# Performance work log

Measured on AMD Instinct MI355X. Metric: run time of the kernel, lower is better.

## Reference

```python
import jax, jax.numpy as jnp
import numpy as np
import math

B, T, D, H = 4, 2048, 1024, 16
HD = D // H  # head dim = 64

def setup_inputs() -> dict:
    key = jax.random.key(0)
    ks = jax.random.split(key, 4)
    scale = 1.0 / math.sqrt(D)
    return {
        "x": jax.random.normal(ks[0], (B, T, D), dtype=jnp.float32),
        "Wq": jax.random.normal(ks[1], (D, D), dtype=jnp.float32) * scale,
        "bq": jnp.zeros((D,), dtype=jnp.float32),
        "Wk": jax.random.normal(ks[2], (D, D), dtype=jnp.float32) * scale,
        "bk": jnp.zeros((D,), dtype=jnp.float32),
        "Wv": jax.random.normal(ks[3], (D, D), dtype=jnp.float32) * scale,
        "bv": jnp.zeros((D,), dtype=jnp.float32),
    }

def reference(x, Wq, bq, Wk, bk, Wv, bv):
    b, t, d = x.shape
    # QKV projections (nn.Dense): x @ W + b
    q = x @ Wq + bq
    k = x @ Wk + bk
    v = x @ Wv + bv
    # b n (h d) -> b h n d
    def split_heads(y):
        return y.reshape(b, t, H, HD).transpose(0, 2, 1, 3)
    q, k, v = split_heads(q), split_heads(k), split_heads(v)
    # scaled dot-product attention; scale by sqrt(features // heads)
    scores = jnp.einsum("bhqd,bhkd->bhqk", q, k) / math.sqrt(HD)
    attn = jax.nn.softmax(scores, axis=-1)
    # dropout rate 0.0 / eval mode => identity
    out = jnp.einsum("bhqk,bhkd->bhqd", attn, v)
    # b h n d -> b n (h d)
    return out.transpose(0, 2, 1, 3).reshape(b, t, d)
```

## Files before the change

### kernel.cpp

```cpp
#include <hip/hip_runtime.h>
#include <math.h>

typedef unsigned short u16;
typedef short short8 __attribute__((ext_vector_type(8)));
typedef short short4v __attribute__((ext_vector_type(4)));
typedef u16 u16x4 __attribute__((ext_vector_type(4)));
typedef float f32x4 __attribute__((ext_vector_type(4)));
typedef __bf16 bf16x8 __attribute__((ext_vector_type(8)));
typedef __bf16 bf16x4 __attribute__((ext_vector_type(4)));

#define B_ 4
#define T_ 2048
#define D_ 1024
#define H_ 16
#define HD_ 64
#define BT_ 8192

__device__ __forceinline__ u16 f2bf(float f) {
  unsigned u = __builtin_bit_cast(unsigned, f);
  u = u + 0x7fffu + ((u >> 16) & 1u);
  return (u16)(u >> 16);
}
__device__ __forceinline__ f32x4 mfma16(short8 a, short8 b, f32x4 c) {
  return __builtin_amdgcn_mfma_f32_16x16x32_bf16(
      __builtin_bit_cast(bf16x8, a), __builtin_bit_cast(bf16x8, b), c, 0, 0, 0);
}
#if __has_builtin(__builtin_amdgcn_mfma_f32_16x16x16bf16_1k)
__device__ __forceinline__ f32x4 mfma_pv(short4v p, short4v v, f32x4 c) {
  return __builtin_amdgcn_mfma_f32_16x16x16bf16_1k(
      __builtin_bit_cast(bf16x4, p), __builtin_bit_cast(bf16x4, v), c, 0, 0, 0);
}
#else
__device__ __forceinline__ f32x4 mfma_pv(short4v p, short4v v, f32x4 c) {
  short8 a = {p[0], p[1], p[2], p[3], 0, 0, 0, 0};
  short8 b = {v[0], v[1], v[2], v[3], 0, 0, 0, 0};
  return mfma16(a, b, c);
}
#endif
__device__ __forceinline__ void async16(u16* lds, const u16* g) {
  __builtin_amdgcn_global_load_lds(
      (const __attribute__((address_space(1))) unsigned int*)g,
      (__attribute__((address_space(3))) unsigned int*)lds, 16, 0, 0);
}
__device__ __forceinline__ short4v pack4(float p0, float p1, float p2, float p3) {
  bf16x4 t = {(__bf16)p0, (__bf16)p1, (__bf16)p2, (__bf16)p3};
  return __builtin_bit_cast(short4v, t);
}

__global__ __launch_bounds__(256) void convert_x(const float* __restrict__ in,
                                                 u16* __restrict__ out) {
  int i = (blockIdx.x * 256 + threadIdx.x) * 4;
  float4 v = *(const float4*)&in[i];
  u16x4 o = {f2bf(v.x), f2bf(v.y), f2bf(v.z), f2bf(v.w)};
  *(u16x4*)&out[i] = o;
}

__global__ __launch_bounds__(256) void transposeW3(
    const float* __restrict__ Wq, const float* __restrict__ Wk,
    const float* __restrict__ Wv, u16* __restrict__ wtq, u16* __restrict__ wtk,
    u16* __restrict__ wtv) {
  __shared__ float sh[32][33];
  const int wsel = blockIdx.y >> 5;
  const float* in = (wsel == 0) ? Wq : (wsel == 1) ? Wk : Wv;
  u16* out = (wsel == 0) ? wtq : (wsel == 1) ? wtk : wtv;
  const int bx = blockIdx.x * 32, by = (blockIdx.y & 31) * 32;
  const int col = threadIdx.x & 31, r8 = threadIdx.x >> 5;
#pragma unroll
  for (int i = 0; i < 4; i++) {
    int row = r8 + i * 8;
    sh[row][col] = in[(size_t)(by + row) * 1024 + bx + col];
  }
  __syncthreads();
#pragma unroll
  for (int i = 0; i < 4; i++) {
    int row = r8 + i * 8;
    out[(size_t)(bx + row) * 1024 + by + col] = f2bf(sh[col][row]);
  }
}

__global__ __launch_bounds__(256, 3) void gemm_qkv3(
    const u16* __restrict__ xbf, const u16* __restrict__ wtq,
    const u16* __restrict__ wtk, const u16* __restrict__ wtv,
    const float* __restrict__ bq, const float* __restrict__ bk,
    const float* __restrict__ bv, u16* __restrict__ qh, u16* __restrict__ kh,
    u16* __restrict__ vth, float qscale) {
  __shared__ __align__(16) u16 Rs[128 * 64];
  __shared__ __align__(16) u16 Cs[128 * 64];
  const int proj = blockIdx.y >> 3;
  const int fy = blockIdx.y & 7;
  const u16* Rm;
  const u16* Cm;
  const float* bias;
  u16* out;
  float scale;
  int r0, c0, vmode;
  if (proj == 0) {
    Rm = wtq; Cm = xbf; bias = bq; out = qh; scale = qscale; vmode = 0;
    r0 = fy * 128; c0 = blockIdx.x * 128;
  } else if (proj == 1) {
    Rm = wtk; Cm = xbf; bias = bk; out = kh; scale = 1.0f; vmode = 0;
    r0 = fy * 128; c0 = blockIdx.x * 128;
  } else {
    Rm = xbf; Cm = wtv; bias = bv; out = vth; scale = 1.0f; vmode = 1;
    r0 = blockIdx.x * 128; c0 = fy * 128;
  }
  const int tid = threadIdx.x;
  const int lane = tid & 63;
  const int w = tid >> 6;
  const int wr = w >> 1, wc = w & 1;
  const int c = lane & 15, q4 = lane >> 4;
  const int cx7 = c & 7;

  f32x4 acc[4][4];
#pragma unroll
  for (int i = 0; i < 4; i++)
#pragma unroll
    for (int j = 0; j < 4; j++) {
      f32x4 z = {0.f, 0.f, 0.f, 0.f};
      acc[i][j] = z;
    }

  const int sr = tid >> 3, pc = tid & 7;

  for (int kk = 0; kk < 1024; kk += 64) {
    __syncthreads();
#pragma unroll
    for (int i = 0; i < 4; i++) {
      int row = i * 32 + sr;
      int sc = (pc ^ (row & 7)) * 8;
      async16(&Rs[(i * 256 + tid) * 8], &Rm[(size_t)(r0 + row) * 1024 + kk + sc]);
      async16(&Cs[(i * 256 + tid) * 8], &Cm[(size_t)(c0 + row) * 1024 + kk + sc]);
    }
    __syncthreads();
#pragma unroll
    for (int h = 0; h < 2; h++) {
      short8 rF[4], cF[4];
      const int ko = ((h * 4 + q4) ^ cx7) * 8;
#pragma unroll
      for (int i = 0; i < 4; i++)
        rF[i] = *(const short8*)&Rs[(wr * 64 + i * 16 + c) * 64 + ko];
#pragma unroll
      for (int j = 0; j < 4; j++)
        cF[j] = *(const short8*)&Cs[(wc * 64 + j * 16 + c) * 64 + ko];
#pragma unroll
      for (int i = 0; i < 4; i++)
#pragma unroll
        for (int j = 0; j < 4; j++) acc[i][j] = mfma16(rF[i], cF[j], acc[i][j]);
    }
  }

  if (vmode == 0) {
#pragma unroll
    for (int i = 0; i < 4; i++) {
      int ng = r0 + wr * 64 + i * 16 + q4 * 4;
      int h = ng >> 6, hd = ng & 63;
#pragma unroll
      for (int j = 0; j < 4; j++) {
        int tg = c0 + wc * 64 + j * 16 + c;
        int b = tg >> 11, tt = tg & 2047;
        u16x4 o;
#pragma unroll
        for (int r = 0; r < 4; r++)
          o[r] = f2bf((acc[i][j][r] + bias[ng + r]) * scale);
        *(u16x4*)&out[(((size_t)(b * 16 + h) * 2048 + tt) << 6) + hd] = o;
      }
    }
  } else {
#pragma unroll
    for (int i = 0; i < 4; i++) {
      int tg = r0 + wr * 64 + i * 16 + q4 * 4;
      int b = tg >> 11, tt = tg & 2047;
#pragma unroll
      for (int j = 0; j < 4; j++) {
        int ng = c0 + wc * 64 + j * 16 + c;
        int h = ng >> 6, hd = ng & 63;
        float bb = bias[ng];
        u16x4 o;
#pragma unroll
        for (int r = 0; r < 4; r++) o[r] = f2bf(acc[i][j][r] + bb);
        *(u16x4*)&out[((size_t)((b * 16 + h) * 64 + hd)) * 2048 + tt] = o;
      }
    }
  }
}

__global__ __launch_bounds__(256, 4) void attn_fused(const u16* __restrict__ Qh,
                                                     const u16* __restrict__ Kh,
                                                     const u16* __restrict__ VTh,
                                                     float* __restrict__ out) {
  __shared__ __align__(16) u16 Ks[2][64 * 64];
  __shared__ __align__(16) u16 VTs[2][64 * 64];
  const int tid = threadIdx.x;
  const int w = tid >> 6, lane = tid & 63;
  const int c = lane & 15, q4 = lane >> 4;
  const int cx7 = c & 7;
  const int qt = blockIdx.x, bh = blockIdx.y;

  short8 qf[2][2];
#pragma unroll
  for (int nblk = 0; nblk < 2; nblk++) {
    const u16* Qp =
        Qh + ((size_t)bh * T_ + qt * 128 + w * 32 + nblk * 16 + c) * 64;
    qf[nblk][0] = *(const short8*)&Qp[q4 * 8];
    qf[nblk][1] = *(const short8*)&Qp[32 + q4 * 8];
  }

  const u16* Kb = Kh + (size_t)bh * T_ * 64;
  const u16* Vb = VTh + (size_t)bh * 64 * T_;

  f32x4 O[2][4];
#pragma unroll
  for (int nblk = 0; nblk < 2; nblk++)
#pragma unroll
    for (int nb = 0; nb < 4; nb++) {
      f32x4 z = {0.f, 0.f, 0.f, 0.f};
      O[nblk][nb] = z;
    }
  float lsum[2] = {0.f, 0.f};

  const int sr = tid >> 3, pc = tid & 7;

#pragma unroll
  for (int i = 0; i < 2; i++) {
    int r = i * 32 + sr;
    int sc = (pc ^ (r & 7)) * 8;
    async16(&Ks[0][(i * 256 + tid) * 8], &Kb[(size_t)r * 64 + sc]);
    async16(&VTs[0][(i * 256 + tid) * 8], &Vb[(size_t)r * T_ + sc]);
  }

  for (int it = 0; it < T_ / 64; it++) {
    const int cur = it & 1;
    __syncthreads();
    if (it + 1 < T_ / 64) {
      const int kt = (it + 1) * 64;
#pragma unroll
      for (int i = 0; i < 2; i++) {
        int r = i * 32 + sr;
        int sc = (pc ^ (r & 7)) * 8;
        async16(&Ks[cur ^ 1][(i * 256 + tid) * 8],
                &Kb[(size_t)(kt + r) * 64 + sc]);
        async16(&VTs[cur ^ 1][(i * 256 + tid) * 8],
                &Vb[(size_t)r * T_ + kt + sc]);
      }
    }

    f32x4 S[4][2];
#pragma unroll
    for (int kb = 0; kb < 4; kb++) {
      short8 k0 =
          *(const short8*)&Ks[cur][(kb * 16 + c) * 64 + ((q4 ^ cx7) * 8)];
      short8 k1 =
          *(const short8*)&Ks[cur][(kb * 16 + c) * 64 + (((4 + q4) ^ cx7) * 8)];
#pragma unroll
      for (int nblk = 0; nblk < 2; nblk++) {
        f32x4 z = {0.f, 0.f, 0.f, 0.f};
        S[kb][nblk] = mfma16(k0, qf[nblk][0], z);
        S[kb][nblk] = mfma16(k1, qf[nblk][1], S[kb][nblk]);
      }
    }

    short4v pf[2][4];
#pragma unroll
    for (int nblk = 0; nblk < 2; nblk++) {
      float rs = 0.f;
#pragma unroll
      for (int kb = 0; kb < 4; kb++) {
        float p0 = __builtin_amdgcn_exp2f(S[kb][nblk][0]);
        float p1 = __builtin_amdgcn_exp2f(S[kb][nblk][1]);
        float p2 = __builtin_amdgcn_exp2f(S[kb][nblk][2]);
        float p3 = __builtin_amdgcn_exp2f(S[kb][nblk][3]);
        rs += (p0 + p1) + (p2 + p3);
        pf[nblk][kb] = pack4(p0, p1, p2, p3);
      }
      lsum[nblk] += rs;
    }

#pragma unroll
    for (int kb = 0; kb < 4; kb++) {
      int pch = ((kb * 2 + (q4 >> 1)) ^ cx7) * 8 + (q4 & 1) * 4;
#pragma unroll
      for (int nb = 0; nb < 4; nb++) {
        short4v vf = *(const short4v*)&VTs[cur][(nb * 16 + c) * 64 + pch];
        O[0][nb] = mfma_pv(pf[0][kb], vf, O[0][nb]);
        O[1][nb] = mfma_pv(pf[1][kb], vf, O[1][nb]);
      }
    }
  }

#pragma unroll
  for (int nblk = 0; nblk < 2; nblk++) {
    lsum[nblk] += __shfl_xor(lsum[nblk], 16);
    lsum[nblk] += __shfl_xor(lsum[nblk], 32);
  }

  const int bq = bh >> 4, h = bh & 15;
#pragma unroll
  for (int nblk = 0; nblk < 2; nblk++)
#pragma unroll
    for (int r = 0; r < 4; r++) {
      float rl = 1.0f / __shfl(lsum[nblk], q4 * 4 + r);
      int t = qt * 128 + w * 32 + nblk * 16 + q4 * 4 + r;
#pragma unroll
      for (int nb = 0; nb < 4; nb++)
        out[((size_t)(bq * T_ + t)) * 1024 + h * 64 + nb * 16 + c] =
            O[nblk][nb][r] * rl;
    }
}

extern "C" void kernel_launch(void* const* d_in, const int* in_sizes, int n_in,
                              void* d_out, int out_size, void* d_ws, size_t ws_size,
                              hipStream_t stream) {
  (void)in_sizes; (void)n_in; (void)out_size; (void)ws_size;
  const float* x  = (const float*)d_in[0];
  const float* Wq = (const float*)d_in[1];
  const float* bq = (const float*)d_in[2];
  const float* Wk = (const float*)d_in[3];
  const float* bk = (const float*)d_in[4];
  const float* Wv = (const float*)d_in[5];
  const float* bv = (const float*)d_in[6];
  float* out = (float*)d_out;

  u16* ob  = (u16*)d_out;
  u16* xbf = ob;
  u16* wtq = ob + (size_t)BT_ * D_;
  u16* wtk = wtq + (size_t)D_ * D_;
  u16* wtv = wtk + (size_t)D_ * D_;

  u16* ws  = (u16*)d_ws;
  u16* qh  = ws;
  u16* kh  = qh + (size_t)BT_ * D_;
  u16* vth = kh + (size_t)BT_ * D_;

  convert_x<<<8192, 256, 0, stream>>>(x, xbf);
  transposeW3<<<dim3(32, 96), 256, 0, stream>>>(Wq, Wk, Wv, wtq, wtk, wtv);

  const float qscale = 0.125f * 1.44269504088896f;
  gemm_qkv3<<<dim3(64, 24), 256, 0, stream>>>(xbf, wtq, wtk, wtv, bq, bk, bv,
                                              qh, kh, vth, qscale);

  attn_fused<<<dim3(16, 64), 256, 0, stream>>>(qh, kh, vth, out);
}
```

Before: 263.7 us.

## Double query rows per attention block and use K=32 MFMA for PV

```diff
diff --git a/kernel.cpp b/kernel.cpp
--- a/kernel.cpp
+++ b/kernel.cpp
@@ -3,11 +3,9 @@
 
 typedef unsigned short u16;
 typedef short short8 __attribute__((ext_vector_type(8)));
-typedef short short4v __attribute__((ext_vector_type(4)));
 typedef u16 u16x4 __attribute__((ext_vector_type(4)));
 typedef float f32x4 __attribute__((ext_vector_type(4)));
 typedef __bf16 bf16x8 __attribute__((ext_vector_type(8)));
-typedef __bf16 bf16x4 __attribute__((ext_vector_type(4)));
 
 #define B_ 4
 #define T_ 2048
@@ -25,26 +23,10 @@
   return __builtin_amdgcn_mfma_f32_16x16x32_bf16(
       __builtin_bit_cast(bf16x8, a), __builtin_bit_cast(bf16x8, b), c, 0, 0, 0);
 }
-#if __has_builtin(__builtin_amdgcn_mfma_f32_16x16x16bf16_1k)
-__device__ __forceinline__ f32x4 mfma_pv(short4v p, short4v v, f32x4 c) {
-  return __builtin_amdgcn_mfma_f32_16x16x16bf16_1k(
-      __builtin_bit_cast(bf16x4, p), __builtin_bit_cast(bf16x4, v), c, 0, 0, 0);
-}
-#else
-__device__ __forceinline__ f32x4 mfma_pv(short4v p, short4v v, f32x4 c) {
-  short8 a = {p[0], p[1], p[2], p[3], 0, 0, 0, 0};
-  short8 b = {v[0], v[1], v[2], v[3], 0, 0, 0, 0};
-  return mfma16(a, b, c);
-}
-#endif
 __device__ __forceinline__ void async16(u16* lds, const u16* g) {
   __builtin_amdgcn_global_load_lds(
       (const __attribute__((address_space(1))) unsigned int*)g,
       (__attribute__((address_space(3))) unsigned int*)lds, 16, 0, 0);
-}
-__device__ __forceinline__ short4v pack4(float p0, float p1, float p2, float p3) {
-  bf16x4 t = {(__bf16)p0, (__bf16)p1, (__bf16)p2, (__bf16)p3};
-  return __builtin_bit_cast(short4v, t);
 }
 
 __global__ __launch_bounds__(256) void convert_x(const float* __restrict__ in,
@@ -170,6 +152,7 @@
     for (int i = 0; i < 4; i++) {
       int tg = r0 + wr * 64 + i * 16 + q4 * 4;
       int b = tg >> 11, tt = tg & 2047;
+      int tp = (tt & ~63) | (((tt >> 2) & 3) << 4) | (((tt >> 4) & 3) << 2);
 #pragma unroll
       for (int j = 0; j < 4; j++) {
         int ng = c0 + wc * 64 + j * 16 + c;
@@ -178,13 +161,13 @@
         u16x4 o;
 #pragma unroll
         for (int r = 0; r < 4; r++) o[r] = f2bf(acc[i][j][r] + bb);
-        *(u16x4*)&out[((size_t)((b * 16 + h) * 64 + hd)) * 2048 + tt] = o;
-      }
-    }
-  }
-}
-
-__global__ __launch_bounds__(256, 4) void attn_fused(const u16* __restrict__ Qh,
+        *(u16x4*)&out[((size_t)((b * 16 + h) * 64 + hd)) * 2048 + tp] = o;
+      }
+    }
+  }
+}
+
+__global__ __launch_bounds__(256, 2) void attn_fused(const u16* __restrict__ Qh,
                                                      const u16* __restrict__ Kh,
                                                      const u16* __restrict__ VTh,
                                                      float* __restrict__ out) {
@@ -196,11 +179,11 @@
   const int cx7 = c & 7;
   const int qt = blockIdx.x, bh = blockIdx.y;
 
-  short8 qf[2][2];
-#pragma unroll
-  for (int nblk = 0; nblk < 2; nblk++) {
+  short8 qf[4][2];
+#pragma unroll
+  for (int nblk = 0; nblk < 4; nblk++) {
     const u16* Qp =
-        Qh + ((size_t)bh * T_ + qt * 128 + w * 32 + nblk * 16 + c) * 64;
+        Qh + ((size_t)bh * T_ + qt * 256 + w * 64 + nblk * 16 + c) * 64;
     qf[nblk][0] = *(const short8*)&Qp[q4 * 8];
     qf[nblk][1] = *(const short8*)&Qp[32 + q4 * 8];
   }
@@ -208,15 +191,15 @@
   const u16* Kb = Kh + (size_t)bh * T_ * 64;
   const u16* Vb = VTh + (size_t)bh * 64 * T_;
 
-  f32x4 O[2][4];
-#pragma unroll
-  for (int nblk = 0; nblk < 2; nblk++)
+  f32x4 O[4][4];
+#pragma unroll
+  for (int nblk = 0; nblk < 4; nblk++)
 #pragma unroll
     for (int nb = 0; nb < 4; nb++) {
       f32x4 z = {0.f, 0.f, 0.f, 0.f};
       O[nblk][nb] = z;
     }
-  float lsum[2] = {0.f, 0.f};
+  float lsum[4] = {0.f, 0.f, 0.f, 0.f};
 
   const int sr = tid >> 3, pc = tid & 7;
 
@@ -244,62 +227,64 @@
       }
     }
 
-    f32x4 S[4][2];
-#pragma unroll
-    for (int kb = 0; kb < 4; kb++) {
-      short8 k0 =
-          *(const short8*)&Ks[cur][(kb * 16 + c) * 64 + ((q4 ^ cx7) * 8)];
-      short8 k1 =
-          *(const short8*)&Ks[cur][(kb * 16 + c) * 64 + (((4 + q4) ^ cx7) * 8)];
-#pragma unroll
-      for (int nblk = 0; nblk < 2; nblk++) {
-        f32x4 z = {0.f, 0.f, 0.f, 0.f};
-        S[kb][nblk] = mfma16(k0, qf[nblk][0], z);
-        S[kb][nblk] = mfma16(k1, qf[nblk][1], S[kb][nblk]);
-      }
-    }
-
-    short4v pf[2][4];
-#pragma unroll
-    for (int nblk = 0; nblk < 2; nblk++) {
-      float rs = 0.f;
-#pragma unroll
-      for (int kb = 0; kb < 4; kb++) {
-        float p0 = __builtin_amdgcn_exp2f(S[kb][nblk][0]);
-        float p1 = __builtin_amdgcn_exp2f(S[kb][nblk][1]);
-        float p2 = __builtin_amdgcn_exp2f(S[kb][nblk][2]);
-        float p3 = __builtin_amdgcn_exp2f(S[kb][nblk][3]);
-        rs += (p0 + p1) + (p2 + p3);
-        pf[nblk][kb] = pack4(p0, p1, p2, p3);
-      }
-      lsum[nblk] += rs;
-    }
-
-#pragma unroll
-    for (int kb = 0; kb < 4; kb++) {
-      int pch = ((kb * 2 + (q4 >> 1)) ^ cx7) * 8 + (q4 & 1) * 4;
+#pragma unroll
+    for (int p = 0; p < 2; p++) {
+      f32x4 S[2][4];
+#pragma unroll
+      for (int kbi = 0; kbi < 2; kbi++) {
+        const int kb = p * 2 + kbi;
+        short8 k0 =
+            *(const short8*)&Ks[cur][(kb * 16 + c) * 64 + ((q4 ^ cx7) * 8)];
+        short8 k1 = *(const short8*)&Ks[cur][(kb * 16 + c) * 64 +
+                                             (((4 + q4) ^ cx7) * 8)];
+#pragma unroll
+        for (int nblk = 0; nblk < 4; nblk++) {
+          f32x4 z = {0.f, 0.f, 0.f, 0.f};
+          S[kbi][nblk] = mfma16(k0, qf[nblk][0], z);
+          S[kbi][nblk] = mfma16(k1, qf[nblk][1], S[kbi][nblk]);
+        }
+      }
+
+      short8 pf8[4];
+#pragma unroll
+      for (int nblk = 0; nblk < 4; nblk++) {
+        float e[8];
+#pragma unroll
+        for (int kbi = 0; kbi < 2; kbi++)
+#pragma unroll
+          for (int r = 0; r < 4; r++)
+            e[kbi * 4 + r] = __builtin_amdgcn_exp2f(S[kbi][nblk][r]);
+        lsum[nblk] += ((e[0] + e[1]) + (e[2] + e[3])) +
+                      ((e[4] + e[5]) + (e[6] + e[7]));
+        bf16x8 t = {(__bf16)e[0], (__bf16)e[1], (__bf16)e[2], (__bf16)e[3],
+                    (__bf16)e[4], (__bf16)e[5], (__bf16)e[6], (__bf16)e[7]};
+        pf8[nblk] = __builtin_bit_cast(short8, t);
+      }
+
 #pragma unroll
       for (int nb = 0; nb < 4; nb++) {
-        short4v vf = *(const short4v*)&VTs[cur][(nb * 16 + c) * 64 + pch];
-        O[0][nb] = mfma_pv(pf[0][kb], vf, O[0][nb]);
-        O[1][nb] = mfma_pv(pf[1][kb], vf, O[1][nb]);
-      }
-    }
-  }
-
-#pragma unroll
-  for (int nblk = 0; nblk < 2; nblk++) {
+        short8 vf = *(const short8*)&VTs[cur][(nb * 16 + c) * 64 +
+                                              (((q4 * 2 + p) ^ cx7) * 8)];
+#pragma unroll
+        for (int nblk = 0; nblk < 4; nblk++)
+          O[nblk][nb] = mfma16(pf8[nblk], vf, O[nblk][nb]);
+      }
+    }
+  }
+
+#pragma unroll
+  for (int nblk = 0; nblk < 4; nblk++) {
     lsum[nblk] += __shfl_xor(lsum[nblk], 16);
     lsum[nblk] += __shfl_xor(lsum[nblk], 32);
   }
 
   const int bq = bh >> 4, h = bh & 15;
 #pragma unroll
-  for (int nblk = 0; nblk < 2; nblk++)
+  for (int nblk = 0; nblk < 4; nblk++)
 #pragma unroll
     for (int r = 0; r < 4; r++) {
       float rl = 1.0f / __shfl(lsum[nblk], q4 * 4 + r);
-      int t = qt * 128 + w * 32 + nblk * 16 + q4 * 4 + r;
+      int t = qt * 256 + w * 64 + nblk * 16 + q4 * 4 + r;
 #pragma unroll
       for (int nb = 0; nb < 4; nb++)
         out[((size_t)(bq * T_ + t)) * 1024 + h * 64 + nb * 16 + c] =
@@ -338,5 +323,5 @@
   gemm_qkv3<<<dim3(64, 24), 256, 0, stream>>>(xbf, wtq, wtk, wtv, bq, bk, bv,
                                               qh, kh, vth, qscale);
 
-  attn_fused<<<dim3(16, 64), 256, 0, stream>>>(qh, kh, vth, out);
-}
+  attn_fused<<<dim3(8, 64), 256, 0, stream>>>(qh, kh, vth, out);
+}
```

Result: faster. 234.0 us (-11.2%).
